# Kernel tuning notes

Hardware: AMD Instinct MI355X
Metric: run time of the kernel (lower is better)

Reference implementation:

```python
import jax, jax.numpy as jnp
import numpy as np

# dims: batch, samples, agents, obs_dim, action_dim, hidden
B, S, N, D, A, H = 512, 64, 8, 64, 16, 256
IN_DIM = (D + A) * N  # 640


def mish(x):
    return x * jnp.tanh(jax.nn.softplus(x))


def setup_inputs() -> dict:
    key = jax.random.key(0)
    ks = jax.random.split(key, 9)
    u = lambda k, shape, fan_in: jax.random.uniform(
        k, shape, jnp.float32, -1.0 / np.sqrt(fan_in), 1.0 / np.sqrt(fan_in))
    return {
        "state": jax.random.normal(ks[0], (B, N, D), jnp.float32),
        "action": jax.random.normal(ks[1], (B, N, A), jnp.float32),
        "W1": u(ks[2], (IN_DIM, H), IN_DIM),
        "b1": u(ks[3], (H,), IN_DIM),
        "W2": u(ks[4], (H, H), H),
        "b2": u(ks[5], (H,), H),
        "W3": u(ks[6], (H, 1), H),
        "b3": u(ks[7], (1,), H),
        # random grand-coalition permutations of the N agents, per (batch, sample)
        "perm": jnp.argsort(jax.random.uniform(ks[8], (B, S, N)), axis=-1).astype(jnp.int32),
    }


def reference(state, action, W1, b1, W2, b2, W3, b3, perm):
    # subcoalition mask [B,S,N,N]: torch builds one-hot(perm) @ tril(ones),
    # i.e. mask[b,s,i,j] = 1 iff j <= perm[b,s,i]
    subcoal = (jnp.arange(N) <= perm[..., None]).astype(state.dtype)
    # gathered actions in coalition order [B,S,N,A]: act_g[b,s,j] = action[b, perm[b,s,j]]
    act_g = action[jnp.arange(B)[:, None, None], perm]
    # masked subcoalition actions [B,S,N,N,A] -> [B,S,N,N*A]
    act = (act_g[:, :, None, :, :] * subcoal[..., None]).reshape(B, S, N, N * A)
    # flattened global obs broadcast over (sample, agent) axes [B,S,N,N*D]
    obs = jnp.broadcast_to(state.reshape(B, 1, 1, N * D), (B, S, N, N * D))
    x = jnp.concatenate([obs, act], axis=-1)  # [B,S,N,IN_DIM]
    # per-agent loop in torch uses shared q1 weights -> single batched MLP
    h = mish(x @ W1 + b1)
    h = mish(h @ W2 + b2)
    q = h @ W3 + b3                   # [B,S,N,1]
    q1 = q.mean(axis=1).squeeze(-1)   # mean over samples -> [B,N]
    return (q1, q1)
```

## Files before the change

kernel.cpp:

```cpp
#include <hip/hip_runtime.h>
#include <hip/hip_bf16.h>

typedef unsigned short ushort_t;
typedef __attribute__((ext_vector_type(8))) short short8;
typedef __attribute__((ext_vector_type(4))) float floatx4;


__device__ __forceinline__ float mish_f(float x) {
    float e = __expf(x);
    float w = fmaf(e, e + 2.0f, 2.0f);
    return x - 2.0f * x * __builtin_amdgcn_rcpf(w);
}

__device__ __forceinline__ unsigned f2bf_u(float f) {
    unsigned int u = __float_as_uint(f);
    return (u + 0x7fffu + ((u >> 16) & 1u)) >> 16;
}

__global__ __launch_bounds__(256) void prep_kernel(
        const float* __restrict__ state,
        const float* __restrict__ action,
        const float* __restrict__ W1,
        const float* __restrict__ b1,
        const float* __restrict__ W2,
        float* __restrict__ obsW,
        ushort_t* __restrict__ actW,
        ushort_t* __restrict__ W2T) {
    int bid = blockIdx.x;
    int t = threadIdx.x;
    if (bid < 512) {
        int b = bid;
        const float* stp = state + (size_t)b * 512;
        const float* w1p = W1 + t;
        float a0 = 0.f, a1 = 0.f, a2 = 0.f, a3 = 0.f;
#pragma unroll 8
        for (int f = 0; f < 512; f += 4) {
            a0 = fmaf(stp[f + 0], w1p[(f + 0) * 256], a0);
            a1 = fmaf(stp[f + 1], w1p[(f + 1) * 256], a1);
            a2 = fmaf(stp[f + 2], w1p[(f + 2) * 256], a2);
            a3 = fmaf(stp[f + 3], w1p[(f + 3) * 256], a3);
        }
        obsW[b * 256 + t] = (a0 + a1) + (a2 + a3) + b1[t];
    } else if (bid < 4608) {
        int idx = bid - 512;
        int b = idx >> 3;
        int j = idx & 7;
        const float* acp = action + (size_t)b * 128;
        const float* W1a = W1 + (size_t)(512 + j * 16) * 256;
        float acc[8];
#pragma unroll
        for (int n = 0; n < 8; ++n) acc[n] = 0.f;
#pragma unroll
        for (int a = 0; a < 16; ++a) {
            float w = W1a[a * 256 + t];
#pragma unroll
            for (int n = 0; n < 8; ++n)
                acc[n] = fmaf(acp[n * 16 + a], w, acc[n]);
        }
#pragma unroll
        for (int n = 0; n < 8; ++n)
            actW[(((size_t)b * 8 + n) * 8 + j) * 256 + t] = (ushort_t)f2bf_u(acc[n]);
    } else {
        int n = (bid - 4608) * 4 + (t >> 6);
        int klo = (t & 63);
        for (int kk = 0; kk < 4; ++kk) {
            int k = kk * 64 + klo;
            W2T[n * 256 + k] = (ushort_t)f2bf_u(W2[k * 256 + n]);
        }
    }
}

#define LDK 264

__global__ __launch_bounds__(512, 8) void main_kernel(
        const float* __restrict__ obsW, const ushort_t* __restrict__ actW,
        const ushort_t* __restrict__ W2T, const int* __restrict__ perm,
        const float* __restrict__ b2,
        const float* __restrict__ W3, const float* __restrict__ b3,
        float* __restrict__ out) {
    __shared__ ushort_t h1[64 * LDK];
    __shared__ float obsb[256];
    __shared__ int perm_s[64];
    __shared__ float qpart[8][64];
    __shared__ float qv_s[64];

    int t = threadIdx.x;
    int bid = blockIdx.x;
    int b = (bid & 7) * 64 + ((bid >> 3) & 63);
    int sg = bid >> 9;
    int s0 = sg * 8;

    if (t < 256) obsb[t] = obsW[b * 256 + t];
    else if (t < 320) perm_s[t - 256] = perm[((size_t)b * 64 + s0) * 8 + (t - 256)];
    __syncthreads();

    const ushort_t* actb = actW + (size_t)b * 64 * 256;
    {
        int slg = t >> 7;
        int c = (t & 127) * 2;
        float ob0 = obsb[c], ob1 = obsb[c + 1];
#pragma unroll
        for (int sl2 = 0; sl2 < 2; ++sl2) {
            int sl = slg * 2 + sl2;
            unsigned av[8];
#pragma unroll
            for (int j = 0; j < 8; ++j) {
                int p = perm_s[sl * 8 + j];
                av[j] = *reinterpret_cast<const unsigned*>(actb + (p * 8 + j) * 256 + c);
            }
            float r0 = ob0, r1 = ob1;
#pragma unroll
            for (int j = 0; j < 8; ++j) {
                r0 += __uint_as_float(av[j] << 16);
                r1 += __uint_as_float(av[j] & 0xffff0000u);
                __hip_bfloat162 pk = __float22bfloat162_rn(make_float2(mish_f(r0), mish_f(r1)));
                *reinterpret_cast<__hip_bfloat162*>(&h1[(sl * 8 + j) * LDK + c]) = pk;
            }
        }
    }
    __syncthreads();

    int w = t >> 6;
    int L = t & 63;
    int lo = L & 15;
    int q = L >> 4;

    floatx4 acc[4][2];
#pragma unroll
    for (int mt = 0; mt < 4; ++mt)
#pragma unroll
        for (int nt = 0; nt < 2; ++nt)
            acc[mt][nt] = (floatx4){0.f, 0.f, 0.f, 0.f};

    const ushort_t* w2base = W2T + ((size_t)(w * 32 + lo)) * 256 + q * 8;

#pragma unroll
    for (int ks = 0; ks < 8; ++ks) {
        short8 afr[4];
#pragma unroll
        for (int mt = 0; mt < 4; ++mt)
            afr[mt] = *reinterpret_cast<const short8*>(&h1[(mt * 16 + lo) * LDK + ks * 32 + q * 8]);
#pragma unroll
        for (int nt = 0; nt < 2; ++nt) {
            short8 bfr = *reinterpret_cast<const short8*>(w2base + nt * 16 * 256 + ks * 32);
#pragma unroll
            for (int mt = 0; mt < 4; ++mt)
                acc[mt][nt] = __builtin_amdgcn_mfma_f32_16x16x32_bf16(afr[mt], bfr, acc[mt][nt], 0, 0, 0);
        }
    }

    float b2c[2], w3c[2];
#pragma unroll
    for (int nt = 0; nt < 2; ++nt) {
        int col = w * 32 + nt * 16 + lo;
        b2c[nt] = b2[col];
        w3c[nt] = W3[col];
    }
#pragma unroll
    for (int mt = 0; mt < 4; ++mt) {
        float part[4] = {0.f, 0.f, 0.f, 0.f};
#pragma unroll
        for (int nt = 0; nt < 2; ++nt) {
#pragma unroll
            for (int r = 0; r < 4; ++r) {
                float h2 = mish_f(acc[mt][nt][r] + b2c[nt]);
                part[r] = fmaf(h2, w3c[nt], part[r]);
            }
        }
#pragma unroll
        for (int r = 0; r < 4; ++r) {
            float v = part[r];
            v += __shfl_xor(v, 1);
            v += __shfl_xor(v, 2);
            v += __shfl_xor(v, 4);
            v += __shfl_xor(v, 8);
            if (lo == 0) qpart[w][mt * 16 + q * 4 + r] = v;
        }
    }
    __syncthreads();
    if (t < 64) {
        float qv = b3[0];
#pragma unroll
        for (int ww = 0; ww < 8; ++ww) qv += qpart[ww][t];
        qv_s[t] = qv;
    }
    __syncthreads();
    if (t < 8) {
        float p = 0.f;
#pragma unroll
        for (int sl = 0; sl < 8; ++sl)
            p += qv_s[sl * 8 + perm_s[sl * 8 + t]];
        p *= (1.0f / 64.0f);
        atomicAdd(&out[b * 8 + t], p);
        atomicAdd(&out[4096 + b * 8 + t], p);
    }
}

extern "C" void kernel_launch(void* const* d_in, const int* in_sizes, int n_in,
                              void* d_out, int out_size, void* d_ws, size_t ws_size,
                              hipStream_t stream) {
    const float* state  = (const float*)d_in[0];
    const float* action = (const float*)d_in[1];
    const float* W1     = (const float*)d_in[2];
    const float* b1     = (const float*)d_in[3];
    const float* W2     = (const float*)d_in[4];
    const float* b2     = (const float*)d_in[5];
    const float* W3     = (const float*)d_in[6];
    const float* b3     = (const float*)d_in[7];
    const int*   perm   = (const int*)d_in[8];
    float* out = (float*)d_out;

    char* ws = (char*)d_ws;
    float*    obsW = (float*)ws;
    ushort_t* actW = (ushort_t*)(ws + 524288);
    ushort_t* W2T  = (ushort_t*)(ws + 524288 + 16777216);

    hipMemsetAsync(out, 0, (size_t)out_size * sizeof(float), stream);
    prep_kernel<<<4672, 256, 0, stream>>>(state, action, W1, b1, W2, obsW, actW, W2T);
    main_kernel<<<4096, 512, 0, stream>>>(obsW, actW, W2T, perm, b2, W3, b3, out);
}
```

Before: 181.8 us.

## Use MFMA-fragment-ordered LDS layout for h1 and prefetch early W2 fragments

Stores the first-layer activations in LDS in 16-row chunks matching the MFMA A-fragment order, so each lane reads one contiguous short8 per fragment. The activation build now has each lane handle four columns with 8-byte gathers and stores instead of two columns. The first two k-steps of W2 fragments are loaded before the first barrier to hide global latency, and launch bounds drop from 8 to 4 blocks per CU, which may change register allocation and occupancy.

```diff
diff --git a/kernel.cpp b/kernel.cpp
--- a/kernel.cpp
+++ b/kernel.cpp
@@ -15,6 +15,10 @@
 __device__ __forceinline__ unsigned f2bf_u(float f) {
     unsigned int u = __float_as_uint(f);
     return (u + 0x7fffu + ((u >> 16) & 1u)) >> 16;
+}
+
+__device__ __forceinline__ unsigned pk_bf2(float a, float b) {
+    return f2bf_u(a) | (f2bf_u(b) << 16);
 }
 
 __global__ __launch_bounds__(256) void prep_kernel(
@@ -70,16 +74,16 @@
     }
 }
 
-#define LDK 264
-
-__global__ __launch_bounds__(512, 8) void main_kernel(
+#define CHUNK_US 528
+
+__global__ __launch_bounds__(512, 4) void main_kernel(
         const float* __restrict__ obsW, const ushort_t* __restrict__ actW,
         const ushort_t* __restrict__ W2T, const int* __restrict__ perm,
         const float* __restrict__ b2,
         const float* __restrict__ W3, const float* __restrict__ b3,
         float* __restrict__ out) {
-    __shared__ ushort_t h1[64 * LDK];
-    __shared__ float obsb[256];
+    __shared__ __align__(16) ushort_t h1[32 * CHUNK_US];
+    __shared__ __align__(16) float obsb[256];
     __shared__ int perm_s[64];
     __shared__ float qpart[8][64];
     __shared__ float qv_s[64];
@@ -90,41 +94,55 @@
     int sg = bid >> 9;
     int s0 = sg * 8;
 
-    if (t < 256) obsb[t] = obsW[b * 256 + t];
-    else if (t < 320) perm_s[t - 256] = perm[((size_t)b * 64 + s0) * 8 + (t - 256)];
-    __syncthreads();
-
-    const ushort_t* actb = actW + (size_t)b * 64 * 256;
-    {
-        int slg = t >> 7;
-        int c = (t & 127) * 2;
-        float ob0 = obsb[c], ob1 = obsb[c + 1];
-#pragma unroll
-        for (int sl2 = 0; sl2 < 2; ++sl2) {
-            int sl = slg * 2 + sl2;
-            unsigned av[8];
-#pragma unroll
-            for (int j = 0; j < 8; ++j) {
-                int p = perm_s[sl * 8 + j];
-                av[j] = *reinterpret_cast<const unsigned*>(actb + (p * 8 + j) * 256 + c);
-            }
-            float r0 = ob0, r1 = ob1;
-#pragma unroll
-            for (int j = 0; j < 8; ++j) {
-                r0 += __uint_as_float(av[j] << 16);
-                r1 += __uint_as_float(av[j] & 0xffff0000u);
-                __hip_bfloat162 pk = __float22bfloat162_rn(make_float2(mish_f(r0), mish_f(r1)));
-                *reinterpret_cast<__hip_bfloat162*>(&h1[(sl * 8 + j) * LDK + c]) = pk;
-            }
-        }
-    }
-    __syncthreads();
-
     int w = t >> 6;
     int L = t & 63;
     int lo = L & 15;
     int q = L >> 4;
 
+    if (t < 256) obsb[t] = obsW[b * 256 + t];
+    else if (t < 320) perm_s[t - 256] = perm[((size_t)b * 64 + s0) * 8 + (t - 256)];
+
+    const ushort_t* w2base = W2T + ((size_t)(w * 32 + lo)) * 256 + q * 8;
+    short8 bpre[4];
+    bpre[0] = *reinterpret_cast<const short8*>(w2base + 0 * 16 * 256 + 0 * 32);
+    bpre[1] = *reinterpret_cast<const short8*>(w2base + 1 * 16 * 256 + 0 * 32);
+    bpre[2] = *reinterpret_cast<const short8*>(w2base + 0 * 16 * 256 + 1 * 32);
+    bpre[3] = *reinterpret_cast<const short8*>(w2base + 1 * 16 * 256 + 1 * 32);
+
+    __syncthreads();
+
+    {
+        int sl = w;
+        int hg = L;
+        int g = hg >> 1;
+        int ks = g >> 2;
+        int qq = g & 3;
+        int half = hg & 1;
+        const ushort_t* actg = actW + (size_t)b * 64 * 256 + hg * 4;
+        uint2 av[8];
+#pragma unroll
+        for (int j = 0; j < 8; ++j) {
+            int p = perm_s[sl * 8 + j];
+            av[j] = *reinterpret_cast<const uint2*>(actg + (p * 8 + j) * 256);
+        }
+        float4 ob = *reinterpret_cast<const float4*>(obsb + hg * 4);
+        float r0 = ob.x, r1 = ob.y, r2 = ob.z, r3 = ob.w;
+        ushort_t* dst0 = h1 + (qq * 16) * 8 + half * 4 + ks * CHUNK_US;
+#pragma unroll
+        for (int j = 0; j < 8; ++j) {
+            r0 += __uint_as_float(av[j].x << 16);
+            r1 += __uint_as_float(av[j].x & 0xffff0000u);
+            r2 += __uint_as_float(av[j].y << 16);
+            r3 += __uint_as_float(av[j].y & 0xffff0000u);
+            int row = sl * 8 + j;
+            int mt = row >> 4, lr = row & 15;
+            uint2 pk = make_uint2(pk_bf2(mish_f(r0), mish_f(r1)),
+                                  pk_bf2(mish_f(r2), mish_f(r3)));
+            *reinterpret_cast<uint2*>(dst0 + mt * 8 * CHUNK_US + lr * 8) = pk;
+        }
+    }
+    __syncthreads();
+
     floatx4 acc[4][2];
 #pragma unroll
     for (int mt = 0; mt < 4; ++mt)
@@ -132,17 +150,20 @@
         for (int nt = 0; nt < 2; ++nt)
             acc[mt][nt] = (floatx4){0.f, 0.f, 0.f, 0.f};
 
-    const ushort_t* w2base = W2T + ((size_t)(w * 32 + lo)) * 256 + q * 8;
+    const ushort_t* h1b = h1 + L * 8;
 
 #pragma unroll
     for (int ks = 0; ks < 8; ++ks) {
         short8 afr[4];
 #pragma unroll
         for (int mt = 0; mt < 4; ++mt)
-            afr[mt] = *reinterpret_cast<const short8*>(&h1[(mt * 16 + lo) * LDK + ks * 32 + q * 8]);
+            afr[mt] = *reinterpret_cast<const short8*>(h1b + (mt * 8 + ks) * CHUNK_US);
 #pragma unroll
         for (int nt = 0; nt < 2; ++nt) {
-            short8 bfr = *reinterpret_cast<const short8*>(w2base + nt * 16 * 256 + ks * 32);
+            short8 bfr;
+            if (ks == 0)      bfr = bpre[nt];
+            else if (ks == 1) bfr = bpre[2 + nt];
+            else              bfr = *reinterpret_cast<const short8*>(w2base + nt * 16 * 256 + ks * 32);
 #pragma unroll
             for (int mt = 0; mt < 4; ++mt)
                 acc[mt][nt] = __builtin_amdgcn_mfma_f32_16x16x32_bf16(afr[mt], bfr, acc[mt][nt], 0, 0, 0);
@@ -215,7 +236,7 @@
     ushort_t* actW = (ushort_t*)(ws + 524288);
     ushort_t* W2T  = (ushort_t*)(ws + 524288 + 16777216);
 
-    hipMemsetAsync(out, 0, (size_t)out_size * sizeof(float), stream);
+    (void)hipMemsetAsync(out, 0, (size_t)out_size * sizeof(float), stream);
     prep_kernel<<<4672, 256, 0, stream>>>(state, action, W1, b1, W2, obsW, actW, W2T);
     main_kernel<<<4096, 512, 0, stream>>>(obsW, actW, W2T, perm, b2, W3, b3, out);
 }
```

Measured after the change: 184.6 us. About the same (+1.5%).
